# Kernel optimization log

Measured on AMD Instinct MI355X. Metric: run time of the kernel, lower is better.

The kernel has to match this reference:

```python
import jax, jax.numpy as jnp
import numpy as np


def _cft_icft_matrices(n):
    # Continuous FT over t in [0,1) sampled at n points, frequencies = fftfreq(n, d=1/n).
    # CFT  : X(f) = integral x(t) e^{-2pi i f t} dt  ~=  (1/n) * sum_t x(t) e^{-2pi i f t}
    # ICFT : x(t) = integral X(f) e^{+2pi i f t} df  ~=  df   * sum_f X(f) e^{+2pi i f t}
    # The original module evaluates the ICFT on the fftshift-ed frequency grid while the
    # coefficients stay in fft (unshifted) index order; we reproduce that pairing.
    sr = float(n)
    t = jnp.arange(n, dtype=jnp.float32) / n                      # [n]
    f = jnp.fft.fftfreq(n, d=1.0 / sr).astype(jnp.float32)        # [n], fft order
    f_shift = jnp.fft.fftshift(f)                                 # [n], shifted order
    two_pi = jnp.float32(2.0 * np.pi)
    dt = jnp.float32(1.0 / n)
    df = jnp.float32(sr / n)  # frequency spacing = 1.0 for unit duration
    # E_cft: [n_freq, n_time], E_icft: [n_time, n_freq]
    E_cft = jnp.exp(-1j * two_pi * f[:, None] * t[None, :]).astype(jnp.complex64) * dt
    E_icft = jnp.exp(1j * two_pi * t[:, None] * f_shift[None, :]).astype(jnp.complex64) * df
    return E_cft, E_icft


def setup_inputs() -> dict:
    key = jax.random.key(0)
    k1, k2, k3 = jax.random.split(key, 3)
    B, Ci, Co, n, modes = 32, 64, 64, 4096, 64
    scale = 1.0 / (Ci * Co)
    x = jax.random.normal(k1, (B, Ci, n), dtype=jnp.float32)
    # weights1 = scale * rand(Ci, Co, modes, cfloat): uniform[0,1) real and imag parts
    w_real = scale * jax.random.uniform(k2, (Ci, Co, modes), dtype=jnp.float32)
    w_imag = scale * jax.random.uniform(k3, (Ci, Co, modes), dtype=jnp.float32)
    return {"x": x, "w_real": w_real, "w_imag": w_imag}


def reference(x, w_real, w_imag):
    B, Ci, n = x.shape
    Co, modes = w_real.shape[1], w_real.shape[2]
    E_cft, E_icft = _cft_icft_matrices(n)
    w = (w_real + 1j * w_imag).astype(jnp.complex64)              # [Ci, Co, modes]
    xc = x.astype(jnp.complex64)
    # Batched CFT over all (batch, channel) pairs as one complex GEMM.
    x_cft = jnp.einsum('bit,ft->bif', xc, E_cft)                  # [B, Ci, n]
    # Spectral linear transform on the lowest `modes` frequencies.
    low = jnp.einsum('bif,iof->bof', x_cft[:, :, :modes], w)      # [B, Co, modes]
    out_ft = jnp.zeros((B, Co, n), dtype=jnp.complex64).at[:, :, :modes].set(low)
    # Batched ICFT back to the time grid; module returns the real part.
    out = jnp.einsum('bof,tf->bot', out_ft, E_icft)               # [B, Co, n]
    return out.real
```

## Files before the change

kernel.cpp:

```cpp
#include <hip/hip_runtime.h>
#include <math.h>

#define NT 4096
#define MODES 64
#define ROWS 2048
#define TWO_PI 6.283185307179586f

typedef __attribute__((ext_vector_type(8))) short bf16x8;
typedef __attribute__((ext_vector_type(4))) float f32x4;

static __device__ __forceinline__ void rotm(float& wr, float& wi, float sr, float si) {
  float nr = fmaf(wr, sr, -wi * si);
  float ni = fmaf(wr, si,  wi * sr);
  wr = nr; wi = ni;
}

static __device__ __forceinline__ unsigned short bf16rn(float x) {
  unsigned u = __float_as_uint(x);
  u += 0x7FFFu + ((u >> 16) & 1u);
  return (unsigned short)(u >> 16);
}

__global__ __launch_bounds__(256) void bgen_kernel(unsigned short* __restrict__ Bg) {
  const int e0 = ((int)blockIdx.x * 256 + (int)threadIdx.x) * 8;
  const int n = e0 >> 12;
  const int t0 = e0 & 4095;
  const int k = (n < 64) ? n : (n - 64);
  bf16x8 pack;
#pragma unroll
  for (int j = 0; j < 8; ++j) {
    const int ph = (k * (t0 + j)) & (NT - 1);
    float s, c;
    sincosf(TWO_PI * (float)ph / (float)NT, &s, &c);
    const float v = ((n < 64) ? c : -s) * (1.0f / (float)NT);
    pack[j] = (short)bf16rn(v);
  }
  *(bf16x8*)(Bg + e0) = pack;
}

__global__ __launch_bounds__(256) void cft_mfma_kernel(
    const float* __restrict__ x, const unsigned short* __restrict__ Bg,
    float* __restrict__ xfp,
    const float* __restrict__ w_real, const float* __restrict__ w_imag,
    float* __restrict__ wrt, float* __restrict__ wit, int S) {
  __shared__ __align__(16) char smem[24576];
  const int tid = threadIdx.x;
  const int nCft = 64 * S;

  if ((int)blockIdx.x >= nCft) {
    float (*tile)[65] = (float (*)[65])smem;
    const int bx = (int)blockIdx.x - nCft;
    const int sel = bx >> 6;
    const int io0 = (bx & 63) * 64;
    const float* __restrict__ src = sel ? w_imag : w_real;
    float* __restrict__ dst = sel ? wit : wrt;
#pragma unroll
    for (int j = 0; j < 4; ++j) {
      const int idx = tid + j * 256;
      const int r = idx >> 4;
      const int kq = idx & 15;
      float4 v = ((const float4*)src)[(size_t)(io0 + r) * 16 + kq];
      tile[r][4 * kq + 0] = v.x; tile[r][4 * kq + 1] = v.y;
      tile[r][4 * kq + 2] = v.z; tile[r][4 * kq + 3] = v.w;
    }
    __syncthreads();
#pragma unroll
    for (int j = 0; j < 16; ++j) {
      const int idx = tid + j * 256;
      const int k = idx >> 6;
      const int r = idx & 63;
      dst[(size_t)k * 4096 + io0 + r] = tile[r][k];
    }
    return;
  }

  unsigned short* Ah = (unsigned short*)smem;
  unsigned short* Al = (unsigned short*)(smem + 4096);
  unsigned short* Bs = (unsigned short*)(smem + 8192);

  const int rowblk = (int)blockIdx.x / S;
  const int ts = (int)blockIdx.x % S;
  const int row0 = rowblk * 32;
  const int t0 = ts * (NT / S);
  const int subs = (NT / S) / 64;

  const int lane = tid & 63;
  const int w = tid >> 6;

  f32x4 acc[2][2];
#pragma unroll
  for (int mt = 0; mt < 2; ++mt)
#pragma unroll
    for (int nt = 0; nt < 2; ++nt) acc[mt][nt] = (f32x4){0.f, 0.f, 0.f, 0.f};

  const int aru = tid & 7;
  const int arow = tid >> 3;

  for (int sub = 0; sub < subs; ++sub) {
    const int tb = t0 + sub * 64;
    __syncthreads();
    {
      const float* xp = x + (size_t)(row0 + arow) * NT + tb + aru * 8;
      const float4 v0 = *(const float4*)xp;
      const float4 v1 = *(const float4*)(xp + 4);
      float xv[8] = {v0.x, v0.y, v0.z, v0.w, v1.x, v1.y, v1.z, v1.w};
      bf16x8 ph, pl;
#pragma unroll
      for (int j = 0; j < 8; ++j) {
        const unsigned short h = bf16rn(xv[j]);
        ph[j] = (short)h;
        const float hf = __uint_as_float((unsigned)h << 16);
        pl[j] = (short)bf16rn(xv[j] - hf);
      }
      const int col = (aru ^ (arow & 7)) * 8;
      *(bf16x8*)(Ah + arow * 64 + col) = ph;
      *(bf16x8*)(Al + arow * 64 + col) = pl;
    }
#pragma unroll
    for (int it = 0; it < 4; ++it) {
      const int idx = tid + it * 256;
      const int ku = idx & 7;
      const int n = idx >> 3;
      const bf16x8 v = *(const bf16x8*)(Bg + (size_t)n * NT + tb + ku * 8);
      const int col = (ku ^ (n & 7)) * 8;
      *(bf16x8*)(Bs + n * 64 + col) = v;
    }
    __syncthreads();
    const int kg = lane >> 4;
#pragma unroll
    for (int ks = 0; ks < 2; ++ks) {
      bf16x8 bf[2];
#pragma unroll
      for (int nt = 0; nt < 2; ++nt) {
        const int n = w * 32 + nt * 16 + (lane & 15);
        const int col = ((ks * 4 + kg) ^ (n & 7)) * 8;
        bf[nt] = *(const bf16x8*)(Bs + n * 64 + col);
      }
#pragma unroll
      for (int mt = 0; mt < 2; ++mt) {
        const int row = mt * 16 + (lane & 15);
        const int col = ((ks * 4 + kg) ^ (row & 7)) * 8;
        const bf16x8 ah = *(const bf16x8*)(Ah + row * 64 + col);
        const bf16x8 al = *(const bf16x8*)(Al + row * 64 + col);
#pragma unroll
        for (int nt = 0; nt < 2; ++nt) {
          acc[mt][nt] = __builtin_amdgcn_mfma_f32_16x16x32_bf16(ah, bf[nt], acc[mt][nt], 0, 0, 0);
          acc[mt][nt] = __builtin_amdgcn_mfma_f32_16x16x32_bf16(al, bf[nt], acc[mt][nt], 0, 0, 0);
        }
      }
    }
  }
  const int nb = w * 32 + (lane & 15);
#pragma unroll
  for (int nt = 0; nt < 2; ++nt) {
    const int n = nb + nt * 16;
    const int plane = n >> 6;
    const int kk = n & 63;
#pragma unroll
    for (int mt = 0; mt < 2; ++mt) {
      const int rl = mt * 16 + (lane >> 4) * 4;
      float4 st = {acc[mt][nt][0], acc[mt][nt][1], acc[mt][nt][2], acc[mt][nt][3]};
      ((float4*)xfp)[((((size_t)ts * 64 + rowblk) * 2 + plane) * 64 + kk) * 8 + (rl >> 2)] = st;
    }
  }
}

__global__ __launch_bounds__(256) void mix_kernel(
    const float* __restrict__ wrt, const float* __restrict__ wit,
    const float* __restrict__ xfp, float2* __restrict__ yf_t, int S) {
  __shared__ float2 wsc[4096];
  __shared__ float2 xsh[256];
  const int k = blockIdx.x & 63;
  const int bq = blockIdx.x >> 6;
  const int tid = threadIdx.x;
#pragma unroll
  for (int j = 0; j < 4; ++j) {
    const int idx = tid + 256 * j;
    float4 vr = ((const float4*)(wrt + (size_t)k * 4096))[idx];
    float4 vi = ((const float4*)(wit + (size_t)k * 4096))[idx];
    wsc[4 * idx + 0] = make_float2(vr.x, vi.x);
    wsc[4 * idx + 1] = make_float2(vr.y, vi.y);
    wsc[4 * idx + 2] = make_float2(vr.z, vi.z);
    wsc[4 * idx + 3] = make_float2(vr.w, vi.w);
  }
  {
    const int R = bq * 256 + tid;
    const int rowblk = R >> 5;
    const int rl = R & 31;
    float2 acc = make_float2(0.f, 0.f);
    for (int s = 0; s < S; ++s) {
      const size_t b0 = (((size_t)s * 64 + rowblk) * 2) * 2048;
      acc.x += xfp[b0 + (size_t)k * 32 + rl];
      acc.y += xfp[b0 + 2048 + (size_t)k * 32 + rl];
    }
    xsh[tid] = acc;
  }
  __syncthreads();
  const int o = tid & 63;
  const int bl = tid >> 6;
  float accr = 0.f, acci = 0.f;
#pragma unroll 8
  for (int i = 0; i < 64; ++i) {
    const float2 xv = xsh[bl * 64 + i];
    const float2 w = wsc[i * 64 + o];
    accr = fmaf(xv.x, w.x, accr); accr = fmaf(-xv.y, w.y, accr);
    acci = fmaf(xv.x, w.y, acci); acci = fmaf( xv.y, w.x, acci);
  }
  yf_t[(size_t)k * ROWS + bq * 256 + bl * 64 + o] = make_float2(accr, acci);
}

__global__ __launch_bounds__(256) void icft_kernel(const float2* __restrict__ yf_t,
                                                   float* __restrict__ out) {
  __shared__ float2 ysh[4][66];
  const int rgrp = blockIdx.x >> 1;
  const int tc = blockIdx.x & 1;
  const int row0 = rgrp * 4;
  const int tid = threadIdx.x;
  {
    const int k = tid >> 2;
    const int r = tid & 3;
    ysh[r][k] = yf_t[(size_t)k * ROWS + row0 + r];
  }
  __syncthreads();
  const int tl = tc * 256 + tid;
  float stepr, stepi;
  sincosf(TWO_PI * (float)tl / (float)NT, &stepi, &stepr);
  float wr = 1.f, wi = 0.f;
  float Gr[8][4] = {{0.f}};
  float Gi[8][4] = {{0.f}};
  for (int m = 0; m < 8; ++m) {
#pragma unroll
    for (int cc = 0; cc < 8; ++cc) {
      const int k = 8 * m + cc;
#pragma unroll
      for (int r = 0; r < 4; ++r) {
        const float2 y = ysh[r][k];
        Gr[cc][r] = fmaf(y.x, wr, Gr[cc][r]);
        Gr[cc][r] = fmaf(-y.y, wi, Gr[cc][r]);
        if (cc != 0 && cc != 4) {
          Gi[cc][r] = fmaf(y.x, wi, Gi[cc][r]);
          Gi[cc][r] = fmaf(y.y, wr, Gi[cc][r]);
        }
      }
      rotm(wr, wi, stepr, stepi);
    }
  }
  const float KK = 0.7071067811865476f;
  const float sgn = (tl & 1) ? -1.f : 1.f;
#pragma unroll
  for (int r = 0; r < 4; ++r) {
    const float Ae = (Gr[0][r] + Gr[2][r]) + (Gr[4][r] + Gr[6][r]);
    const float Ao = (Gr[1][r] + Gr[3][r]) + (Gr[5][r] + Gr[7][r]);
    const float A2 = (Gr[0][r] - Gr[2][r]) + (Gr[4][r] - Gr[6][r]);
    const float B2 = (Gi[1][r] - Gi[3][r]) + (Gi[5][r] - Gi[7][r]);
    const float P  = Gr[0][r] - Gr[4][r];
    const float Qr = (Gr[1][r] - Gr[3][r]) - (Gr[5][r] - Gr[7][r]);
    const float R  = Gi[6][r] - Gi[2][r];
    const float Qi = (Gi[5][r] - Gi[1][r]) + (Gi[7][r] - Gi[3][r]);
    const float U = P + R, V = P - R;
    const float W1 = KK * (Qr + Qi), W2 = KK * (Qr - Qi);
    float* op = out + (size_t)(row0 + r) * NT + tl;
    op[0]    = sgn * (Ae + Ao);
    op[512]  = sgn * (U + W1);
    op[1024] = sgn * (A2 - B2);
    op[1536] = sgn * (V - W2);
    op[2048] = sgn * (Ae - Ao);
    op[2560] = sgn * (U - W1);
    op[3072] = sgn * (A2 + B2);
    op[3584] = sgn * (V + W2);
  }
}

extern "C" void kernel_launch(void* const* d_in, const int* in_sizes, int n_in,
                              void* d_out, int out_size, void* d_ws, size_t ws_size,
                              hipStream_t stream) {
  const float* x      = (const float*)d_in[0];
  const float* w_real = (const float*)d_in[1];
  const float* w_imag = (const float*)d_in[2];
  float* out = (float*)d_out;

  const size_t MB = (size_t)ROWS * MODES * sizeof(float2);
  int S = 16;
  while (S > 4 && (size_t)(S + 5) * MB > ws_size) S >>= 1;

  char* wsp = (char*)d_ws;
  float*  xfp  = (float*)wsp;
  float2* yf_t = (float2*)(wsp + (size_t)S * MB);
  float*  wrt  = (float*)(wsp + (size_t)(S + 2) * MB);
  float*  wit  = (float*)(wsp + (size_t)(S + 3) * MB);
  unsigned short* Bg = (unsigned short*)(wsp + (size_t)(S + 4) * MB);

  bgen_kernel<<<256, 256, 0, stream>>>(Bg);
  cft_mfma_kernel<<<64 * S + 128, 256, 0, stream>>>(x, Bg, xfp, w_real, w_imag,
                                                    wrt, wit, S);
  mix_kernel<<<512, 256, 0, stream>>>(wrt, wit, xfp, yf_t, S);
  icft_kernel<<<1024, 256, 0, stream>>>(yf_t, out);
}
```

Before: 46.00 us.

## Replace scalar ICFT with bf16 MFMA GEMM using precomputed twiddle matrix

The inverse transform now runs on bf16 MFMA instructions against a precomputed cos/sin basis matrix (Cg) generated in the existing basis kernel, instead of a per-thread twiddle recurrence with a radix-8 split. Spectral coefficients are converted to bf16 and stored in swizzled LDS, and basis tiles are staged through LDS per 64-column sub-block. This moves the FMA-heavy ICFT onto matrix cores. In exchange it adds extra basis generation and workspace, and bf16 rounding of both coefficients and basis reduces accuracy.

```diff
diff --git a/kernel.cpp b/kernel.cpp
--- a/kernel.cpp
+++ b/kernel.cpp
@@ -9,33 +9,48 @@
 typedef __attribute__((ext_vector_type(8))) short bf16x8;
 typedef __attribute__((ext_vector_type(4))) float f32x4;
 
-static __device__ __forceinline__ void rotm(float& wr, float& wi, float sr, float si) {
-  float nr = fmaf(wr, sr, -wi * si);
-  float ni = fmaf(wr, si,  wi * sr);
-  wr = nr; wi = ni;
-}
-
 static __device__ __forceinline__ unsigned short bf16rn(float x) {
   unsigned u = __float_as_uint(x);
   u += 0x7FFFu + ((u >> 16) & 1u);
   return (unsigned short)(u >> 16);
 }
 
-__global__ __launch_bounds__(256) void bgen_kernel(unsigned short* __restrict__ Bg) {
-  const int e0 = ((int)blockIdx.x * 256 + (int)threadIdx.x) * 8;
-  const int n = e0 >> 12;
-  const int t0 = e0 & 4095;
-  const int k = (n < 64) ? n : (n - 64);
-  bf16x8 pack;
-#pragma unroll
-  for (int j = 0; j < 8; ++j) {
-    const int ph = (k * (t0 + j)) & (NT - 1);
-    float s, c;
-    sincosf(TWO_PI * (float)ph / (float)NT, &s, &c);
-    const float v = ((n < 64) ? c : -s) * (1.0f / (float)NT);
-    pack[j] = (short)bf16rn(v);
-  }
-  *(bf16x8*)(Bg + e0) = pack;
+__global__ __launch_bounds__(256) void bgen_kernel(unsigned short* __restrict__ Bg,
+                                                   unsigned short* __restrict__ Cg) {
+  const int bx = (int)blockIdx.x;
+  if (bx < 256) {
+    const int e0 = (bx * 256 + (int)threadIdx.x) * 8;
+    const int n = e0 >> 12;
+    const int t0 = e0 & 4095;
+    const int k = (n < 64) ? n : (n - 64);
+    bf16x8 pack;
+#pragma unroll
+    for (int j = 0; j < 8; ++j) {
+      const int ph = (k * (t0 + j)) & (NT - 1);
+      float s, c;
+      sincosf(TWO_PI * (float)ph / (float)NT, &s, &c);
+      const float v = ((n < 64) ? c : -s) * (1.0f / (float)NT);
+      pack[j] = (short)bf16rn(v);
+    }
+    *(bf16x8*)(Bg + e0) = pack;
+  } else {
+    const int e0 = ((bx - 256) * 256 + (int)threadIdx.x) * 8;
+    const int t = e0 >> 7;
+    const int k2b = e0 & 127;
+    const float sgn = (t & 1) ? -1.f : 1.f;
+    bf16x8 pack;
+#pragma unroll
+    for (int j = 0; j < 8; ++j) {
+      const int k2 = k2b + j;
+      const int k = (k2 < 64) ? k2 : (k2 - 64);
+      const int ph = (k * t) & (NT - 1);
+      float s, c;
+      sincosf(TWO_PI * (float)ph / (float)NT, &s, &c);
+      const float v = ((k2 < 64) ? c : -s) * sgn;
+      pack[j] = (short)bf16rn(v);
+    }
+    *(bf16x8*)(Cg + e0) = pack;
+  }
 }
 
 __global__ __launch_bounds__(256) void cft_mfma_kernel(
@@ -209,65 +224,78 @@
   yf_t[(size_t)k * ROWS + bq * 256 + bl * 64 + o] = make_float2(accr, acci);
 }
 
-__global__ __launch_bounds__(256) void icft_kernel(const float2* __restrict__ yf_t,
-                                                   float* __restrict__ out) {
-  __shared__ float2 ysh[4][66];
-  const int rgrp = blockIdx.x >> 1;
-  const int tc = blockIdx.x & 1;
-  const int row0 = rgrp * 4;
+__global__ __launch_bounds__(256) void icft_mfma_kernel(
+    const float2* __restrict__ yf_t, const unsigned short* __restrict__ Cg,
+    float* __restrict__ out) {
+  __shared__ __align__(16) char smem[24576];
+  unsigned short* Ay = (unsigned short*)smem;
+  unsigned short* Cs = (unsigned short*)(smem + 8192);
   const int tid = threadIdx.x;
-  {
-    const int k = tid >> 2;
-    const int r = tid & 3;
-    ysh[r][k] = yf_t[(size_t)k * ROWS + row0 + r];
+  const int rgrp = (int)blockIdx.x >> 4;
+  const int tgrp = (int)blockIdx.x & 15;
+  const int row0 = rgrp * 32;
+  const int tb0 = tgrp * 256;
+  const int lane = tid & 63;
+  const int w = tid >> 6;
+
+#pragma unroll
+  for (int it = 0; it < 8; ++it) {
+    const int idx = tid + it * 256;
+    const int k = idx >> 5;
+    const int rl = idx & 31;
+    const float2 y = yf_t[(size_t)k * ROWS + row0 + rl];
+    const int ur = (k >> 3) ^ (rl & 7);
+    Ay[rl * 128 + ur * 8 + (k & 7)] = bf16rn(y.x);
+    Ay[rl * 128 + (8 | ur) * 8 + (k & 7)] = bf16rn(y.y);
   }
   __syncthreads();
-  const int tl = tc * 256 + tid;
-  float stepr, stepi;
-  sincosf(TWO_PI * (float)tl / (float)NT, &stepi, &stepr);
-  float wr = 1.f, wi = 0.f;
-  float Gr[8][4] = {{0.f}};
-  float Gi[8][4] = {{0.f}};
-  for (int m = 0; m < 8; ++m) {
-#pragma unroll
-    for (int cc = 0; cc < 8; ++cc) {
-      const int k = 8 * m + cc;
-#pragma unroll
-      for (int r = 0; r < 4; ++r) {
-        const float2 y = ysh[r][k];
-        Gr[cc][r] = fmaf(y.x, wr, Gr[cc][r]);
-        Gr[cc][r] = fmaf(-y.y, wi, Gr[cc][r]);
-        if (cc != 0 && cc != 4) {
-          Gi[cc][r] = fmaf(y.x, wi, Gi[cc][r]);
-          Gi[cc][r] = fmaf(y.y, wr, Gi[cc][r]);
-        }
+
+  bf16x8 afr[2][4];
+#pragma unroll
+  for (int mt = 0; mt < 2; ++mt) {
+    const int row = mt * 16 + (lane & 15);
+#pragma unroll
+    for (int ks = 0; ks < 4; ++ks) {
+      const int unit = ks * 4 + (lane >> 4);
+      const int cu = unit ^ (row & 7);
+      afr[mt][ks] = *(const bf16x8*)(Ay + row * 128 + cu * 8);
+    }
+  }
+
+  for (int sub = 0; sub < 4; ++sub) {
+    const int tb = tb0 + sub * 64;
+    __syncthreads();
+#pragma unroll
+    for (int it = 0; it < 4; ++it) {
+      const int idx = tid + it * 256;
+      const int ku = idx & 15;
+      const int tl = idx >> 4;
+      const bf16x8 v = *(const bf16x8*)(Cg + (size_t)(tb + tl) * 128 + ku * 8);
+      Cs[tl * 128 + (ku ^ (tl & 7)) * 8] = 0;
+      *(bf16x8*)(Cs + tl * 128 + (ku ^ (tl & 7)) * 8) = v;
+    }
+    __syncthreads();
+    const int tl = w * 16 + (lane & 15);
+    f32x4 acc[2];
+    acc[0] = (f32x4){0.f, 0.f, 0.f, 0.f};
+    acc[1] = (f32x4){0.f, 0.f, 0.f, 0.f};
+#pragma unroll
+    for (int ks = 0; ks < 4; ++ks) {
+      const int unit = ks * 4 + (lane >> 4);
+      const int cu = unit ^ (tl & 7);
+      const bf16x8 bf = *(const bf16x8*)(Cs + tl * 128 + cu * 8);
+      acc[0] = __builtin_amdgcn_mfma_f32_16x16x32_bf16(afr[0][ks], bf, acc[0], 0, 0, 0);
+      acc[1] = __builtin_amdgcn_mfma_f32_16x16x32_bf16(afr[1][ks], bf, acc[1], 0, 0, 0);
+    }
+    const int t = tb + tl;
+#pragma unroll
+    for (int mt = 0; mt < 2; ++mt) {
+      const int rbase = row0 + mt * 16 + (lane >> 4) * 4;
+#pragma unroll
+      for (int reg = 0; reg < 4; ++reg) {
+        out[(size_t)(rbase + reg) * NT + t] = acc[mt][reg];
       }
-      rotm(wr, wi, stepr, stepi);
-    }
-  }
-  const float KK = 0.7071067811865476f;
-  const float sgn = (tl & 1) ? -1.f : 1.f;
-#pragma unroll
-  for (int r = 0; r < 4; ++r) {
-    const float Ae = (Gr[0][r] + Gr[2][r]) + (Gr[4][r] + Gr[6][r]);
-    const float Ao = (Gr[1][r] + Gr[3][r]) + (Gr[5][r] + Gr[7][r]);
-    const float A2 = (Gr[0][r] - Gr[2][r]) + (Gr[4][r] - Gr[6][r]);
-    const float B2 = (Gi[1][r] - Gi[3][r]) + (Gi[5][r] - Gi[7][r]);
-    const float P  = Gr[0][r] - Gr[4][r];
-    const float Qr = (Gr[1][r] - Gr[3][r]) - (Gr[5][r] - Gr[7][r]);
-    const float R  = Gi[6][r] - Gi[2][r];
-    const float Qi = (Gi[5][r] - Gi[1][r]) + (Gi[7][r] - Gi[3][r]);
-    const float U = P + R, V = P - R;
-    const float W1 = KK * (Qr + Qi), W2 = KK * (Qr - Qi);
-    float* op = out + (size_t)(row0 + r) * NT + tl;
-    op[0]    = sgn * (Ae + Ao);
-    op[512]  = sgn * (U + W1);
-    op[1024] = sgn * (A2 - B2);
-    op[1536] = sgn * (V - W2);
-    op[2048] = sgn * (Ae - Ao);
-    op[2560] = sgn * (U - W1);
-    op[3072] = sgn * (A2 + B2);
-    op[3584] = sgn * (V + W2);
+    }
   }
 }
 
@@ -281,7 +309,7 @@
 
   const size_t MB = (size_t)ROWS * MODES * sizeof(float2);
   int S = 16;
-  while (S > 4 && (size_t)(S + 5) * MB > ws_size) S >>= 1;
+  while (S > 4 && (size_t)(S + 6) * MB > ws_size) S >>= 1;
 
   char* wsp = (char*)d_ws;
   float*  xfp  = (float*)wsp;
@@ -289,10 +317,11 @@
   float*  wrt  = (float*)(wsp + (size_t)(S + 2) * MB);
   float*  wit  = (float*)(wsp + (size_t)(S + 3) * MB);
   unsigned short* Bg = (unsigned short*)(wsp + (size_t)(S + 4) * MB);
-
-  bgen_kernel<<<256, 256, 0, stream>>>(Bg);
+  unsigned short* Cg = (unsigned short*)(wsp + (size_t)(S + 5) * MB);
+
+  bgen_kernel<<<512, 256, 0, stream>>>(Bg, Cg);
   cft_mfma_kernel<<<64 * S + 128, 256, 0, stream>>>(x, Bg, xfp, w_real, w_imag,
                                                     wrt, wit, S);
   mix_kernel<<<512, 256, 0, stream>>>(wrt, wit, xfp, yf_t, S);
-  icft_kernel<<<1024, 256, 0, stream>>>(yf_t, out);
-}
+  icft_mfma_kernel<<<1024, 256, 0, stream>>>(yf_t, Cg, out);
+}
```

After: 42.76 us (median of 2 runs). -7.0%, faster.
